# Kernel optimization log

Measured on AMD Instinct MI355X. Metric: run time of the kernel, lower is better.

## Reference

```python
import jax, jax.numpy as jnp
import numpy as np

NUP, NDOWN = 15, 15
NELEC = NUP + NDOWN
NATOMS = 10
NDIM = 3
NBATCH = 512
FEAT = 64   # hidden feature dim
K_RBF = 64  # gaussian RBF expansion size
NLAYERS = 2
RBF_CUT = 8.0


def _build_graphs():
    # elec-elec: upper-tri pairs, each pair -> 2 directed edges (i->j, j->i),
    # matching ree.repeat_interleave(2) edge-distance ordering.
    ii, jj = np.triu_indices(NELEC, k=1)                      # [435]
    ee_src = np.stack([ii, jj], 1).reshape(-1).astype(np.int32)  # [870]
    ee_dst = np.stack([jj, ii], 1).reshape(-1).astype(np.int32)
    ee_types = np.array([0] * NUP + [1] * NDOWN, np.int32)
    # elec-nuc: nodes = [electrons(0..29), atoms(30..39)];
    # ren is transposed to [natoms, nelec] then flattened -> atom-major pair order.
    aa = np.repeat(np.arange(NATOMS), NELEC)
    ee_ = np.tile(np.arange(NELEC), NATOMS)
    en_src = np.stack([ee_, NELEC + aa], 1).reshape(-1).astype(np.int32)  # [600]
    en_dst = np.stack([NELEC + aa, ee_], 1).reshape(-1).astype(np.int32)
    en_types = np.concatenate([np.array([0] * NUP + [1] * NDOWN),
                               2 + np.arange(NATOMS)]).astype(np.int32)
    return ee_src, ee_dst, ee_types, en_src, en_dst, en_types


def setup_inputs() -> dict:
    key = jax.random.key(0)
    ks = jax.random.split(key, 20)
    ee_src, ee_dst, ee_types, en_src, en_dst, en_types = _build_graphs()
    s = 0.1
    inp = {
        "pos": jax.random.normal(ks[0], (NBATCH, NELEC * NDIM), jnp.float32) * 2.0,
        "atoms": jax.random.normal(ks[1], (NATOMS, NDIM), jnp.float32) * 3.0,
        "emb_ee": jax.random.normal(ks[2], (2, FEAT), jnp.float32) * s,
        "wf_ee": jax.random.normal(ks[3], (K_RBF, FEAT), jnp.float32) * s,
        "bf_ee": jnp.zeros((FEAT,), jnp.float32),
        "wl_ee": jax.random.normal(ks[4], (NLAYERS, FEAT, FEAT), jnp.float32) * s,
        "bl_ee": jnp.zeros((NLAYERS, FEAT), jnp.float32),
        "wr_ee": jax.random.normal(ks[5], (FEAT, 1), jnp.float32) * s,
        "br_ee": jnp.zeros((1,), jnp.float32),
        "emb_en": jax.random.normal(ks[6], (2 + NATOMS, FEAT), jnp.float32) * s,
        "wf_en": jax.random.normal(ks[7], (K_RBF, FEAT), jnp.float32) * s,
        "bf_en": jnp.zeros((FEAT,), jnp.float32),
        "wl_en": jax.random.normal(ks[8], (NLAYERS, FEAT, FEAT), jnp.float32) * s,
        "bl_en": jnp.zeros((NLAYERS, FEAT), jnp.float32),
        "wr_en": jax.random.normal(ks[9], (FEAT, 1), jnp.float32) * s,
        "br_en": jnp.zeros((1,), jnp.float32),
        "ee_src": jnp.asarray(ee_src), "ee_dst": jnp.asarray(ee_dst),
        "ee_types": jnp.asarray(ee_types),
        "en_src": jnp.asarray(en_src), "en_dst": jnp.asarray(en_dst),
        "en_types": jnp.asarray(en_types),
    }
    return inp


def _gnn_kernel(types, src, dst, edist, emb, wf, bf, wl, bl, wr, br):
    """MGCN-style interaction net on a batch of identical graphs.
    types [N] int, src/dst [E] int, edist [nb, E] float."""
    nb = edist.shape[0]
    N = types.shape[0]
    centers = jnp.linspace(0.0, RBF_CUT, K_RBF).astype(edist.dtype)
    rbf = jnp.exp(-(edist[..., None] - centers) ** 2)        # [nb, E, K]
    filt = jnp.tanh(rbf @ wf + bf)                           # [nb, E, F]
    h = jnp.broadcast_to(emb[types][None], (nb, N, emb.shape[1]))  # [nb, N, F]
    for l in range(wl.shape[0]):
        m = h[:, src, :] * filt                              # gather + edge filter
        agg = jnp.zeros_like(h).at[:, dst, :].add(m)         # scatter-add messages
        h = h + jnp.tanh(agg @ wl[l] + bl[l])
    return h.sum(axis=1) @ wr + br                           # [nb, 1] readout


def reference(pos, atoms, emb_ee, wf_ee, bf_ee, wl_ee, bl_ee, wr_ee, br_ee,
              emb_en, wf_en, bf_en, wl_en, bl_en, wr_en, br_en,
              ee_src, ee_dst, ee_types, en_src, en_dst, en_types):
    nb = pos.shape[0]
    xyz = pos.reshape(nb, NELEC, NDIM)
    # elec-elec edge distances (src/dst index electron nodes; symmetric so this
    # equals extract_tri_up(...).repeat_interleave(2))
    d_ee = jnp.linalg.norm(xyz[:, ee_src] - xyz[:, ee_dst], axis=-1)   # [nb, 870]
    # elec-nuc: node positions = [electrons; atoms]
    nodepos = jnp.concatenate(
        [xyz, jnp.broadcast_to(atoms[None], (nb, NATOMS, NDIM))], axis=1)
    d_en = jnp.linalg.norm(nodepos[:, en_src] - nodepos[:, en_dst], axis=-1)  # [nb, 600]
    ee_k = _gnn_kernel(ee_types, ee_src, ee_dst, d_ee,
                       emb_ee, wf_ee, bf_ee, wl_ee, bl_ee, wr_ee, br_ee)
    en_k = _gnn_kernel(en_types, en_src, en_dst, d_en,
                       emb_en, wf_en, bf_en, wl_en, bl_en, wr_en, br_en)
    return jnp.exp(ee_k + en_k)   # [nb, 1] Jastrow factor (derivative=0)
```

## Files before the change

kernel.cpp:

```cpp
#include <hip/hip_runtime.h>
#include <math.h>

#define NB      512
#define NELEC   30
#define NATOMS  10
#define NNEN    40
#define FEAT    64
#define KRBF    64
#define BLOCK   512
#define NWAVES  (BLOCK/64)
#define NPEE    435
#define NPEN    300
#define TILE    32
#define TPAD    33

#define EE_H     96
#define EE_AGG   (EE_H + NELEC*FEAT)
#define EE_FT    (EE_AGG + NELEC*FEAT)
#define EE_TOTAL (EE_FT + NPEE*TPAD)
#define EN_H     96
#define EN_AGG   (EN_H + NNEN*FEAT)
#define EN_FT    (EN_AGG + NNEN*FEAT)
#define EN_TOTAL (EN_FT + NPEN*TPAD)

#define KERNEL_ATTRS __attribute__((amdgpu_flat_work_group_size(BLOCK, BLOCK), \
                                    amdgpu_waves_per_eu(4, 4)))

__device__ __forceinline__ int ee_base(int i) { return 29*i - ((i*(i-1))>>1); }

__global__ KERNEL_ATTRS
void ee_kernel(const float* __restrict__ pos,
               const float* __restrict__ emb,
               const float* __restrict__ wf,
               const float* __restrict__ bf,
               const float* __restrict__ wl,
               const float* __restrict__ bl,
               const float* __restrict__ wr,
               const float* __restrict__ br,
               const int*   __restrict__ types,
               double*      __restrict__ kout)
{
    extern __shared__ float sm[];
    float* xyz  = sm;
    float* hS   = sm + EE_H;
    float* aggS = sm + EE_AGG;
    float* fT   = sm + EE_FT;

    const int tid  = threadIdx.x;
    const int b    = blockIdx.x;
    const int lane = tid & 63;
    const int w    = tid >> 6;

    for (int idx = tid; idx < NELEC*3; idx += BLOCK) xyz[idx] = pos[b*NELEC*3 + idx];
    for (int idx = tid; idx < NELEC*FEAT; idx += BLOCK) {
        int n = idx >> 6, f = idx & 63;
        hS[idx] = emb[types[n]*FEAT + f];
    }
    __syncthreads();

    const int p = (tid < NPEE) ? tid : (NPEE - 1);
    float facc[FEAT];
    {
        int i = 0, rem = p;
        while (rem >= NELEC - 1 - i) { rem -= NELEC - 1 - i; ++i; }
        const int j = i + 1 + rem;
        const float dx = xyz[3*i+0] - xyz[3*j+0];
        const float dy = xyz[3*i+1] - xyz[3*j+1];
        const float dz = xyz[3*i+2] - xyz[3*j+2];
        const float dd = sqrtf(dx*dx + dy*dy + dz*dz);

        #pragma unroll
        for (int f = 0; f < FEAT; ++f) facc[f] = bf[f];
        #pragma unroll 2
        for (int k = 0; k < KRBF; ++k) {
            const float ck = (float)((double)k * (8.0/63.0));
            const float t  = dd - ck;
            const float rk = expf(-t*t);
            const float* wrow = wf + k*FEAT;
            #pragma unroll
            for (int f = 0; f < FEAT; ++f) facc[f] = fmaf(rk, wrow[f], facc[f]);
        }
        #pragma unroll
        for (int f = 0; f < FEAT; ++f) facc[f] = tanhf(facc[f]);
    }

    #pragma unroll
    for (int l = 0; l < 2; ++l) {
        const float* wlL = wl + l*FEAT*FEAT;
        const float* blL = bl + l*FEAT;

        #pragma unroll
        for (int t = 0; t < 2; ++t) {
            __syncthreads();
            #pragma unroll
            for (int ff = 0; ff < TILE; ++ff)
                fT[p*TPAD + ff] = facc[t*TILE + ff];
            __syncthreads();

            #pragma unroll
            for (int pass = 0; pass < 2; ++pass) {
                const int idx = tid + pass*BLOCK;
                if (idx < NELEC*TILE) {
                    const int i  = idx >> 5;
                    const int ff = idx & 31;
                    const int f  = t*TILE + ff;
                    float a = 0.f;
                    #pragma unroll
                    for (int j = 0; j < NELEC; ++j) {
                        if (j != i) {
                            int pp = (j < i) ? (ee_base(j) + (i - j - 1))
                                             : (ee_base(i) + (j - i - 1));
                            a = fmaf(hS[j*FEAT + f], fT[pp*TPAD + ff], a);
                        }
                    }
                    aggS[i*FEAT + f] = a;
                }
            }
        }
        __syncthreads();

        for (int i = w; i < NELEC; i += NWAVES) {
            float a2 = 0.f;
            const float4* arow = reinterpret_cast<const float4*>(aggS + i*FEAT);
            #pragma unroll
            for (int k = 0; k < FEAT/4; ++k) {
                float4 av = arow[k];
                a2 = fmaf(av.x, wlL[(4*k+0)*FEAT + lane], a2);
                a2 = fmaf(av.y, wlL[(4*k+1)*FEAT + lane], a2);
                a2 = fmaf(av.z, wlL[(4*k+2)*FEAT + lane], a2);
                a2 = fmaf(av.w, wlL[(4*k+3)*FEAT + lane], a2);
            }
            hS[i*FEAT + lane] += tanhf(a2 + blL[lane]);
        }
        __syncthreads();
    }

    if (w == 0) {
        float s = 0.f;
        #pragma unroll
        for (int n = 0; n < NELEC; ++n) s += hS[n*FEAT + lane];
        double dv = (double)s * (double)wr[lane];
        #pragma unroll
        for (int o = 32; o > 0; o >>= 1) dv += __shfl_xor(dv, o, 64);
        if (lane == 0) kout[b] = dv + (double)br[0];
    }
}

__global__ KERNEL_ATTRS
void en_kernel(const float* __restrict__ pos,
               const float* __restrict__ atoms,
               const float* __restrict__ emb,
               const float* __restrict__ wf,
               const float* __restrict__ bf,
               const float* __restrict__ wl,
               const float* __restrict__ bl,
               const float* __restrict__ wr,
               const float* __restrict__ br,
               const int*   __restrict__ types,
               const double* __restrict__ kin,
               float*       __restrict__ out)
{
    extern __shared__ float sm[];
    float* xyz  = sm;
    float* hS   = sm + EN_H;
    float* aggS = sm + EN_AGG;
    float* fT   = sm + EN_FT;

    const int tid  = threadIdx.x;
    const int b    = blockIdx.x;
    const int lane = tid & 63;
    const int w    = tid >> 6;

    for (int idx = tid; idx < NELEC*3; idx += BLOCK) xyz[idx] = pos[b*NELEC*3 + idx];
    for (int idx = tid; idx < NNEN*FEAT; idx += BLOCK) {
        int n = idx >> 6, f = idx & 63;
        hS[idx] = emb[types[n]*FEAT + f];
    }
    __syncthreads();

    const int p = (tid < NPEN) ? tid : (NPEN - 1);
    float facc[FEAT];
    {
        const int a = p / NELEC;
        const int e = p - a*NELEC;
        const float dx = xyz[3*e+0] - atoms[3*a+0];
        const float dy = xyz[3*e+1] - atoms[3*a+1];
        const float dz = xyz[3*e+2] - atoms[3*a+2];
        const float dd = sqrtf(dx*dx + dy*dy + dz*dz);

        #pragma unroll
        for (int f = 0; f < FEAT; ++f) facc[f] = bf[f];
        #pragma unroll 2
        for (int k = 0; k < KRBF; ++k) {
            const float ck = (float)((double)k * (8.0/63.0));
            const float t  = dd - ck;
            const float rk = expf(-t*t);
            const float* wrow = wf + k*FEAT;
            #pragma unroll
            for (int f = 0; f < FEAT; ++f) facc[f] = fmaf(rk, wrow[f], facc[f]);
        }
        #pragma unroll
        for (int f = 0; f < FEAT; ++f) facc[f] = tanhf(facc[f]);
    }

    #pragma unroll
    for (int l = 0; l < 2; ++l) {
        const float* wlL = wl + l*FEAT*FEAT;
        const float* blL = bl + l*FEAT;

        #pragma unroll
        for (int t = 0; t < 2; ++t) {
            __syncthreads();
            #pragma unroll
            for (int ff = 0; ff < TILE; ++ff)
                fT[p*TPAD + ff] = facc[t*TILE + ff];
            __syncthreads();

            #pragma unroll
            for (int pass = 0; pass < 3; ++pass) {
                const int idx = tid + pass*BLOCK;
                if (idx < NNEN*TILE) {
                    const int n  = idx >> 5;
                    const int ff = idx & 31;
                    const int f  = t*TILE + ff;
                    float a = 0.f;
                    if (n < NELEC) {
                        #pragma unroll
                        for (int at = 0; at < NATOMS; ++at)
                            a = fmaf(hS[(NELEC+at)*FEAT + f],
                                     fT[(at*NELEC + n)*TPAD + ff], a);
                    } else {
                        const int at = n - NELEC;
                        #pragma unroll
                        for (int e2 = 0; e2 < NELEC; ++e2)
                            a = fmaf(hS[e2*FEAT + f],
                                     fT[(at*NELEC + e2)*TPAD + ff], a);
                    }
                    aggS[n*FEAT + f] = a;
                }
            }
        }
        __syncthreads();

        for (int n = w; n < NNEN; n += NWAVES) {
            float a2 = 0.f;
            const float4* arow = reinterpret_cast<const float4*>(aggS + n*FEAT);
            #pragma unroll
            for (int k = 0; k < FEAT/4; ++k) {
                float4 av = arow[k];
                a2 = fmaf(av.x, wlL[(4*k+0)*FEAT + lane], a2);
                a2 = fmaf(av.y, wlL[(4*k+1)*FEAT + lane], a2);
                a2 = fmaf(av.z, wlL[(4*k+2)*FEAT + lane], a2);
                a2 = fmaf(av.w, wlL[(4*k+3)*FEAT + lane], a2);
            }
            hS[n*FEAT + lane] += tanhf(a2 + blL[lane]);
        }
        __syncthreads();
    }

    if (w == 0) {
        float s = 0.f;
        #pragma unroll
        for (int n = 0; n < NNEN; ++n) s += hS[n*FEAT + lane];
        double dv = (double)s * (double)wr[lane];
        #pragma unroll
        for (int o = 32; o > 0; o >>= 1) dv += __shfl_xor(dv, o, 64);
        if (lane == 0) out[b] = (float)exp(dv + (double)br[0] + kin[b]);
    }
}

extern "C" void kernel_launch(void* const* d_in, const int* in_sizes, int n_in,
                              void* d_out, int out_size, void* d_ws, size_t ws_size,
                              hipStream_t stream) {
    const float* pos    = (const float*)d_in[0];
    const float* atoms  = (const float*)d_in[1];
    const float* emb_ee = (const float*)d_in[2];
    const float* wf_ee  = (const float*)d_in[3];
    const float* bf_ee  = (const float*)d_in[4];
    const float* wl_ee  = (const float*)d_in[5];
    const float* bl_ee  = (const float*)d_in[6];
    const float* wr_ee  = (const float*)d_in[7];
    const float* br_ee  = (const float*)d_in[8];
    const float* emb_en = (const float*)d_in[9];
    const float* wf_en  = (const float*)d_in[10];
    const float* bf_en  = (const float*)d_in[11];
    const float* wl_en  = (const float*)d_in[12];
    const float* bl_en  = (const float*)d_in[13];
    const float* wr_en  = (const float*)d_in[14];
    const float* br_en  = (const float*)d_in[15];
    const int*   ee_ty  = (const int*)d_in[18];
    const int*   en_ty  = (const int*)d_in[21];

    double* kws = (double*)d_ws;
    float*  out = (float*)d_out;

    (void)hipFuncSetAttribute((const void*)ee_kernel,
            hipFuncAttributeMaxDynamicSharedMemorySize, EE_TOTAL*(int)sizeof(float));
    (void)hipFuncSetAttribute((const void*)en_kernel,
            hipFuncAttributeMaxDynamicSharedMemorySize, EN_TOTAL*(int)sizeof(float));

    ee_kernel<<<NB, BLOCK, EE_TOTAL*sizeof(float), stream>>>(
        pos, emb_ee, wf_ee, bf_ee, wl_ee, bl_ee, wr_ee, br_ee, ee_ty, kws);
    en_kernel<<<NB, BLOCK, EN_TOTAL*sizeof(float), stream>>>(
        pos, atoms, emb_en, wf_en, bf_en, wl_en, bl_en, wr_en, br_en, en_ty, kws, out);
}
```

Before: 219.4 us.

## Split RBF filter features across two half-blocks with 1024-thread blocks

Doubles the block size to 1024 threads. Each half of the block computes 32 of the 64 filter features per edge, so the per-thread accumulator array is halved and register pressure drops, allowing higher waves-per-EU. The transposed tile store is done by whichever half owns that feature tile, and the aggregation loops now need a single pass. The tradeoffs are duplicated distance and RBF exp computation in both halves, a larger block per CU, and many idle threads during the aggregation phases.

After: 368.6 us. 68.0% more time.

```diff
diff --git a/kernel.cpp b/kernel.cpp
--- a/kernel.cpp
+++ b/kernel.cpp
@@ -7,7 +7,7 @@
 #define NNEN    40
 #define FEAT    64
 #define KRBF    64
-#define BLOCK   512
+#define BLOCK   1024
 #define NWAVES  (BLOCK/64)
 #define NPEE    435
 #define NPEN    300
@@ -24,7 +24,7 @@
 #define EN_TOTAL (EN_FT + NPEN*TPAD)
 
 #define KERNEL_ATTRS __attribute__((amdgpu_flat_work_group_size(BLOCK, BLOCK), \
-                                    amdgpu_waves_per_eu(4, 4)))
+                                    amdgpu_waves_per_eu(8, 8)))
 
 __device__ __forceinline__ int ee_base(int i) { return 29*i - ((i*(i-1))>>1); }
 
@@ -58,8 +58,9 @@
     }
     __syncthreads();
 
-    const int p = (tid < NPEE) ? tid : (NPEE - 1);
-    float facc[FEAT];
+    const int p  = ((tid & 511) < NPEE) ? (tid & 511) : (NPEE - 1);
+    const int hf = __builtin_amdgcn_readfirstlane(tid >> 9);
+    float facc[TILE];
     {
         int i = 0, rem = p;
         while (rem >= NELEC - 1 - i) { rem -= NELEC - 1 - i; ++i; }
@@ -69,52 +70,49 @@
         const float dz = xyz[3*i+2] - xyz[3*j+2];
         const float dd = sqrtf(dx*dx + dy*dy + dz*dz);
 
-        #pragma unroll
-        for (int f = 0; f < FEAT; ++f) facc[f] = bf[f];
+        const float* bfh = bf + hf*TILE;
+        #pragma unroll
+        for (int f = 0; f < TILE; ++f) facc[f] = bfh[f];
         #pragma unroll 2
         for (int k = 0; k < KRBF; ++k) {
             const float ck = (float)((double)k * (8.0/63.0));
             const float t  = dd - ck;
             const float rk = expf(-t*t);
-            const float* wrow = wf + k*FEAT;
+            const float* wrow = wf + k*FEAT + hf*TILE;
             #pragma unroll
-            for (int f = 0; f < FEAT; ++f) facc[f] = fmaf(rk, wrow[f], facc[f]);
-        }
-        #pragma unroll
-        for (int f = 0; f < FEAT; ++f) facc[f] = tanhf(facc[f]);
-    }
-
-    #pragma unroll
+            for (int f = 0; f < TILE; ++f) facc[f] = fmaf(rk, wrow[f], facc[f]);
+        }
+        #pragma unroll
+        for (int f = 0; f < TILE; ++f) facc[f] = tanhf(facc[f]);
+    }
+
     for (int l = 0; l < 2; ++l) {
         const float* wlL = wl + l*FEAT*FEAT;
         const float* blL = bl + l*FEAT;
 
-        #pragma unroll
         for (int t = 0; t < 2; ++t) {
             __syncthreads();
-            #pragma unroll
-            for (int ff = 0; ff < TILE; ++ff)
-                fT[p*TPAD + ff] = facc[t*TILE + ff];
+            if (hf == t) {
+                #pragma unroll
+                for (int ff = 0; ff < TILE; ++ff)
+                    fT[p*TPAD + ff] = facc[ff];
+            }
             __syncthreads();
 
-            #pragma unroll
-            for (int pass = 0; pass < 2; ++pass) {
-                const int idx = tid + pass*BLOCK;
-                if (idx < NELEC*TILE) {
-                    const int i  = idx >> 5;
-                    const int ff = idx & 31;
-                    const int f  = t*TILE + ff;
-                    float a = 0.f;
-                    #pragma unroll
-                    for (int j = 0; j < NELEC; ++j) {
-                        if (j != i) {
-                            int pp = (j < i) ? (ee_base(j) + (i - j - 1))
-                                             : (ee_base(i) + (j - i - 1));
-                            a = fmaf(hS[j*FEAT + f], fT[pp*TPAD + ff], a);
-                        }
+            if (tid < NELEC*TILE) {
+                const int i  = tid >> 5;
+                const int ff = tid & 31;
+                const int f  = t*TILE + ff;
+                float a = 0.f;
+                #pragma unroll
+                for (int j = 0; j < NELEC; ++j) {
+                    if (j != i) {
+                        int pp = (j < i) ? (ee_base(j) + (i - j - 1))
+                                         : (ee_base(i) + (j - i - 1));
+                        a = fmaf(hS[j*FEAT + f], fT[pp*TPAD + ff], a);
                     }
-                    aggS[i*FEAT + f] = a;
                 }
+                aggS[i*FEAT + f] = a;
             }
         }
         __syncthreads();
@@ -178,8 +176,9 @@
     }
     __syncthreads();
 
-    const int p = (tid < NPEN) ? tid : (NPEN - 1);
-    float facc[FEAT];
+    const int p  = ((tid & 511) < NPEN) ? (tid & 511) : (NPEN - 1);
+    const int hf = __builtin_amdgcn_readfirstlane(tid >> 9);
+    float facc[TILE];
     {
         const int a = p / NELEC;
         const int e = p - a*NELEC;
@@ -188,56 +187,53 @@
         const float dz = xyz[3*e+2] - atoms[3*a+2];
         const float dd = sqrtf(dx*dx + dy*dy + dz*dz);
 
-        #pragma unroll
-        for (int f = 0; f < FEAT; ++f) facc[f] = bf[f];
+        const float* bfh = bf + hf*TILE;
+        #pragma unroll
+        for (int f = 0; f < TILE; ++f) facc[f] = bfh[f];
         #pragma unroll 2
         for (int k = 0; k < KRBF; ++k) {
             const float ck = (float)((double)k * (8.0/63.0));
             const float t  = dd - ck;
             const float rk = expf(-t*t);
-            const float* wrow = wf + k*FEAT;
+            const float* wrow = wf + k*FEAT + hf*TILE;
             #pragma unroll
-            for (int f = 0; f < FEAT; ++f) facc[f] = fmaf(rk, wrow[f], facc[f]);
-        }
-        #pragma unroll
-        for (int f = 0; f < FEAT; ++f) facc[f] = tanhf(facc[f]);
-    }
-
-    #pragma unroll
+            for (int f = 0; f < TILE; ++f) facc[f] = fmaf(rk, wrow[f], facc[f]);
+        }
+        #pragma unroll
+        for (int f = 0; f < TILE; ++f) facc[f] = tanhf(facc[f]);
+    }
+
     for (int l = 0; l < 2; ++l) {
         const float* wlL = wl + l*FEAT*FEAT;
         const float* blL = bl + l*FEAT;
 
-        #pragma unroll
         for (int t = 0; t < 2; ++t) {
             __syncthreads();
-            #pragma unroll
-            for (int ff = 0; ff < TILE; ++ff)
-                fT[p*TPAD + ff] = facc[t*TILE + ff];
+            if (hf == t) {
+                #pragma unroll
+                for (int ff = 0; ff < TILE; ++ff)
+                    fT[p*TPAD + ff] = facc[ff];
+            }
             __syncthreads();
 
-            #pragma unroll
-            for (int pass = 0; pass < 3; ++pass) {
-                const int idx = tid + pass*BLOCK;
-                if (idx < NNEN*TILE) {
-                    const int n  = idx >> 5;
-                    const int ff = idx & 31;
-                    const int f  = t*TILE + ff;
-                    float a = 0.f;
-                    if (n < NELEC) {
-                        #pragma unroll
-                        for (int at = 0; at < NATOMS; ++at)
-                            a = fmaf(hS[(NELEC+at)*FEAT + f],
-                                     fT[(at*NELEC + n)*TPAD + ff], a);
-                    } else {
-                        const int at = n - NELEC;
-                        #pragma unroll
-                        for (int e2 = 0; e2 < NELEC; ++e2)
-                            a = fmaf(hS[e2*FEAT + f],
-                                     fT[(at*NELEC + e2)*TPAD + ff], a);
-                    }
-                    aggS[n*FEAT + f] = a;
+            for (int idx = tid; idx < NNEN*TILE; idx += BLOCK) {
+                const int n  = idx >> 5;
+                const int ff = idx & 31;
+                const int f  = t*TILE + ff;
+                float a = 0.f;
+                if (n < NELEC) {
+                    #pragma unroll
+                    for (int at = 0; at < NATOMS; ++at)
+                        a = fmaf(hS[(NELEC+at)*FEAT + f],
+                                 fT[(at*NELEC + n)*TPAD + ff], a);
+                } else {
+                    const int at = n - NELEC;
+                    #pragma unroll
+                    for (int e2 = 0; e2 < NELEC; ++e2)
+                        a = fmaf(hS[e2*FEAT + f],
+                                 fT[(at*NELEC + e2)*TPAD + ff], a);
                 }
+                aggS[n*FEAT + f] = a;
             }
         }
         __syncthreads();
```
